# Performance work log

Measured on AMD Instinct MI355X. Metric: run time of the kernel, lower is better.

Reference implementation:

```python
import jax, jax.numpy as jnp
import numpy as np

B, S, D = 4, 2048, 1024
H = 8
HD = D // H            # 128 head dim
FF = 4096 // H         # 512 per-head expert hidden
E = 8                  # num experts
K = 2                  # top-k
MU, GAMMA = 0.7, 1.0
LN_EPS = 1e-5


def setup_inputs() -> dict:
    key = jax.random.key(0)
    ks = jax.random.split(key, 12)
    sc = lambda *shape: 1.0 / np.sqrt(shape[0])
    return {
        "x": jax.random.normal(ks[0], (B, S, D), jnp.float32),
        "momentum": jnp.zeros((B * S * H, HD), jnp.float32),
        # split proj (input_dim -> input_dim)
        "split_W": jax.random.normal(ks[1], (D, D), jnp.float32) * sc(D),
        "split_b": jnp.zeros((D,), jnp.float32),
        # gate (head_dim -> num_experts)
        "gate_W": jax.random.normal(ks[2], (HD, E), jnp.float32) * sc(HD),
        "gate_b": jnp.zeros((E,), jnp.float32),
        # stacked experts: Linear(HD->FF) ReLU Linear(FF->HD)
        "W1": jax.random.normal(ks[3], (E, HD, FF), jnp.float32) * sc(HD),
        "b1": jnp.zeros((E, FF), jnp.float32),
        "W2": jax.random.normal(ks[4], (E, FF, HD), jnp.float32) * sc(FF),
        "b2": jnp.zeros((E, HD), jnp.float32),
        # layernorm over head_dim
        "ln_g": jnp.ones((HD,), jnp.float32),
        "ln_b": jnp.zeros((HD,), jnp.float32),
        # merge proj
        "merge_W": jax.random.normal(ks[5], (D, D), jnp.float32) * sc(D),
        "merge_b": jnp.zeros((D,), jnp.float32),
    }


def _topk_gate(t, gate_W, gate_b):
    # t: [T, HD] -> dense gate weights [T, E] with only top-K nonzero
    logits = t @ gate_W + gate_b                       # [T, E]
    topv, topi = jax.lax.top_k(logits, K)              # [T, K]
    gates_k = jax.nn.softmax(topv, axis=-1)            # softmax over kept experts
    onehot = jax.nn.one_hot(topi, E, dtype=t.dtype)    # [T, K, E]
    return jnp.einsum("tk,tke->te", gates_k, onehot)   # scatter back


def reference(x, momentum, split_W, split_b, gate_W, gate_b,
              W1, b1, W2, b2, ln_g, ln_b, merge_W, merge_b):
    # split: [B,S,D] -> [B*S*H, HD]
    x_hat = x @ split_W + split_b
    t = x_hat.reshape(B * S * H, HD)

    gates = _topk_gate(t, gate_W, gate_b)              # [T, E]

    # all-experts dense compute (matches the source's per-expert loop)
    h = jax.nn.relu(jnp.einsum("td,edf->etf", t, W1) + b1[:, None, :])  # [E,T,FF]
    eo = jnp.einsum("etf,efd->etd", h, W2) + b2[:, None, :]             # [E,T,HD]
    expert_outputs = jnp.einsum("te,etd->td", gates, eo)                # [T,HD]

    new_momentum = -expert_outputs + MU * momentum
    out = t + GAMMA * new_momentum

    # layernorm over head_dim
    mean = out.mean(-1, keepdims=True)
    var = out.var(-1, keepdims=True)
    out = (out - mean) * jax.lax.rsqrt(var + LN_EPS) * ln_g + ln_b

    # merge: [T,HD] -> [B,S,D] -> linear
    o = out.reshape(B, S, D)
    final = o @ merge_W + merge_b
    return final, new_momentum
```

## Files before the change

kernel.cpp:

```cpp
#include <hip/hip_runtime.h>

#define NBATCH 4
#define NS 2048
#define ND 1024
#define NH 8
#define HD 128
#define NFF 512
#define NE 8
#define NT 65536
#define NBS 8192
#define MU_F 0.7f
#define LN_EPS_F 1e-5f

typedef __attribute__((ext_vector_type(4))) float f32x4;
typedef __attribute__((ext_vector_type(2))) double f64x2;
typedef __attribute__((ext_vector_type(8))) _Float16 f16x8;
typedef __attribute__((ext_vector_type(4))) _Float16 f16x4;
typedef __attribute__((ext_vector_type(2))) _Float16 f16x2;

__device__ __forceinline__ void gload_lds16(const void* g, void* l) {
  __builtin_amdgcn_global_load_lds(
      (const __attribute__((address_space(1))) unsigned int*)g,
      (__attribute__((address_space(3))) unsigned int*)l, 16, 0, 0);
}

__global__ void zero_cnt_kernel(int* cnt) {
  cnt[threadIdx.x] = 0;
}

__global__ void tr_cvt_kernel(const float* __restrict__ in, _Float16* __restrict__ out, int R, int C) {
  __shared__ float tile[32][33];
  int b = blockIdx.z;
  const float* inp = in + (size_t)b * R * C;
  _Float16* outp = out + (size_t)b * R * C;
  int c = blockIdx.x * 32 + threadIdx.x;
  int r0 = blockIdx.y * 32;
  #pragma unroll
  for (int i = 0; i < 4; i++) {
    int r = r0 + threadIdx.y + i * 8;
    tile[threadIdx.y + i * 8][threadIdx.x] = inp[(size_t)r * C + c];
  }
  __syncthreads();
  int rr = r0 + threadIdx.x;
  #pragma unroll
  for (int i = 0; i < 4; i++) {
    int cc = blockIdx.x * 32 + threadIdx.y + i * 8;
    outp[(size_t)cc * R + rr] = (_Float16)tile[threadIdx.x][threadIdx.y + i * 8];
  }
}

__global__ void build_G_kernel(const float* __restrict__ split_W, const float* __restrict__ split_b,
                               const float* __restrict__ gate_W, const float* __restrict__ gate_b,
                               double* __restrict__ G, double* __restrict__ gbias) {
  int idx = blockIdx.x * 256 + threadIdx.x;
  int d = idx >> 6, o = idx & 63, h = o >> 3, e = o & 7;
  double acc = 0.0;
  const float* r0 = split_W + (size_t)d * ND + h * 128;
  #pragma unroll 4
  for (int j = 0; j < 128; j++)
    acc += (double)r0[j] * (double)gate_W[j * 8 + e];
  G[((size_t)(d >> 1) * 64 + o) * 2 + (d & 1)] = acc;
  if (idx < 64) {
    double bacc = 0.0;
    for (int j = 0; j < 128; j++)
      bacc += (double)split_b[h * 128 + j] * (double)gate_W[j * 8 + e];
    gbias[idx] = bacc + (double)gate_b[e];
  }
}

__global__ __launch_bounds__(256) void gate_kernel(const float* __restrict__ x,
    const f64x2* __restrict__ Gx2, const double* __restrict__ gbias,
    _Float16* __restrict__ x_h,
    float* __restrict__ tkw, int* __restrict__ lists, int* __restrict__ cnt) {
  __shared__ f64x2 Gs[32 * 64];
  __shared__ double xsd[16][66];
  __shared__ double lg[16 * 64];
  __shared__ int lcnt[8];
  __shared__ int lbase[8];
  int tid = threadIdx.x, lane = tid & 63, w = tid >> 6;
  int bs0 = blockIdx.x * 16;
  double acc[4];
  #pragma unroll
  for (int r = 0; r < 4; r++) acc[r] = 0.0;
  int xrow = tid >> 4, xc4 = tid & 15;
  const double* xr = &xsd[0][0] + (w * 4) * 66;
  if (tid < 8) lcnt[tid] = 0;

  for (int ch = 0; ch < 16; ch++) {
    __syncthreads();
    float4 xv4 = *(const float4*)(x + (size_t)(bs0 + xrow) * ND + ch * 64 + xc4 * 4);
    f64x2 xa = { (double)xv4.x, (double)xv4.y };
    f64x2 xb = { (double)xv4.z, (double)xv4.w };
    *(f64x2*)&xsd[xrow][xc4 * 4]     = xa;
    *(f64x2*)&xsd[xrow][xc4 * 4 + 2] = xb;
    f16x4 xh = { (_Float16)xv4.x, (_Float16)xv4.y, (_Float16)xv4.z, (_Float16)xv4.w };
    *(f16x4*)(x_h + (size_t)(bs0 + xrow) * ND + ch * 64 + xc4 * 4) = xh;
    #pragma unroll
    for (int j = 0; j < 8; j++) {
      int n = j * 256 + tid;
      gload_lds16(Gx2 + (size_t)ch * 2048 + n, Gs + n);
    }
    __syncthreads();
    #pragma unroll 4
    for (int kp = 0; kp < 32; kp++) {
      f64x2 g = Gs[kp * 64 + lane];
      #pragma unroll
      for (int r = 0; r < 4; r++) {
        f64x2 xv = *(const f64x2*)(xr + r * 66 + kp * 2);
        acc[r] += xv.x * g.x;
        acc[r] += xv.y * g.y;
      }
    }
  }
  double gb = gbias[lane];
  #pragma unroll
  for (int r = 0; r < 4; r++)
    lg[(w * 4 + r) * 64 + lane] = acc[r] + gb;
  __syncthreads();

  int i1 = 0, i2 = 0, token = 0, p1 = 0, p2 = 0;
  if (tid < 128) {
    int row = tid >> 3, h = tid & 7;
    const double* L = lg + row * 64 + h * 8;
    double v1 = L[0];
    #pragma unroll
    for (int e2 = 1; e2 < 8; e2++) if (L[e2] > v1) { v1 = L[e2]; i1 = e2; }
    i2 = -1; double v2 = -1e300;
    #pragma unroll
    for (int e2 = 0; e2 < 8; e2++) if (e2 != i1 && L[e2] > v2) { v2 = L[e2]; i2 = e2; }
    float ex = expf((float)(v2 - v1));
    float den = 1.f + ex;
    float g1 = 1.f / den, g2 = ex / den;
    token = (bs0 + row) * 8 + h;
    tkw[token * 2]     = g1;
    tkw[token * 2 + 1] = g2;
    p1 = atomicAdd(&lcnt[i1], 1);
    p2 = atomicAdd(&lcnt[i2], 1);
  }
  __syncthreads();
  if (tid < 8) lbase[tid] = atomicAdd(cnt + tid * 64, lcnt[tid]);
  __syncthreads();
  if (tid < 128) {
    lists[(size_t)i1 * NT + lbase[i1] + p1] = token * 2;
    lists[(size_t)i2 * NT + lbase[i2] + p2] = token * 2 + 1;
  }
}

__global__ __launch_bounds__(256) void gemm_f16_kernel(
    const _Float16* __restrict__ A, const _Float16* __restrict__ Bt,
    const float* __restrict__ bias, float* __restrict__ Cf, _Float16* __restrict__ Ch,
    int M, int N, int Kd) {
  __shared__ _Float16 As[128 * 32];
  __shared__ _Float16 Bs[128 * 32];
  int tid = threadIdx.x, lane = tid & 63, w = tid >> 6;
  int wr = w >> 1, wc = w & 1;
  int m0 = blockIdx.y * 128, n0 = blockIdx.x * 128;
  f32x4 acc[4][4];
  #pragma unroll
  for (int i = 0; i < 4; i++)
    #pragma unroll
    for (int j = 0; j < 4; j++) acc[i][j] = (f32x4){0.f, 0.f, 0.f, 0.f};
  int srow = lane >> 2, scol = (lane & 3) * 8;
  int fr = lane & 15, ko = (lane >> 4) * 8;
  const _Float16* Ag = A + (size_t)(m0 + srow) * Kd + scol;
  const _Float16* Bg = Bt + (size_t)(n0 + srow) * Kd + scol;

  for (int k0 = 0; k0 < Kd; k0 += 32) {
    #pragma unroll
    for (int j = 0; j < 2; j++) {
      int rb = (w * 2 + j) * 16;
      gload_lds16(Ag + (size_t)rb * Kd + k0, As + rb * 32);
      gload_lds16(Bg + (size_t)rb * Kd + k0, Bs + rb * 32);
    }
    __syncthreads();
    f16x8 af[4], bq[4];
    #pragma unroll
    for (int mi = 0; mi < 4; mi++) af[mi] = *(const f16x8*)(As + (wr * 64 + mi * 16 + fr) * 32 + ko);
    #pragma unroll
    for (int ni = 0; ni < 4; ni++) bq[ni] = *(const f16x8*)(Bs + (wc * 64 + ni * 16 + fr) * 32 + ko);
    __syncthreads();
    #pragma unroll
    for (int mi = 0; mi < 4; mi++)
      #pragma unroll
      for (int ni = 0; ni < 4; ni++)
        acc[mi][ni] = __builtin_amdgcn_mfma_f32_16x16x32_f16(af[mi], bq[ni], acc[mi][ni], 0, 0, 0);
  }
  int rbase = m0 + wr * 64 + ((lane >> 4) << 2);
  int cbase = n0 + wc * 64 + (lane & 15);
  #pragma unroll
  for (int mi = 0; mi < 4; mi++)
    #pragma unroll
    for (int ni = 0; ni < 4; ni++) {
      int cc = cbase + ni * 16;
      float bv = bias ? bias[cc] : 0.f;
      #pragma unroll
      for (int r = 0; r < 4; r++) {
        int rr = rbase + mi * 16 + r;
        float v = acc[mi][ni][r] + bv;
        if (Cf) Cf[(size_t)rr * N + cc] = v;
        if (Ch) Ch[(size_t)rr * N + cc] = (_Float16)v;
      }
    }
}

__global__ __launch_bounds__(512, 2) void expert_kernel(
    const _Float16* __restrict__ t_h, const _Float16* __restrict__ W1t, const _Float16* __restrict__ W2t,
    const float* __restrict__ b1, const float* __restrict__ b2,
    const int* __restrict__ cnt, const int* __restrict__ lists, const float* __restrict__ tkw,
    _Float16* __restrict__ slots) {
  int e = blockIdx.x & 7;
  int m0 = (blockIdx.x >> 3) * 128;
  int count = cnt[e * 64];
  if (m0 >= count) return;
  __shared__ _Float16 ring[3][64 * 128];
  __shared__ _Float16 h_s[128 * 64];
  __shared__ float b1s[NFF];
  __shared__ float b2s[HD];
  __shared__ int alist[128];
  __shared__ float aw[128];
  int tid = threadIdx.x, lane = tid & 63, w = tid >> 6;
  int wr = w >> 1, wc = w & 1;
  int fr = lane & 15, g = lane >> 4;

  if (tid < 128) {
    int idx = m0 + tid;
    int a = (idx < count) ? lists[(size_t)e * NT + idx] : -1;
    alist[tid] = a;
    aw[tid] = (a >= 0) ? tkw[a] : 0.f;
  }
  b1s[tid] = b1[e * NFF + tid];
  if (tid < 128) b2s[tid] = b2[e * HD + tid];
  __syncthreads();

  auto stage = [&](int p) {
    if (p >= 16) return;
    int ch = p >> 1;
    _Float16* dst = &ring[p % 3][0];
    if ((p & 1) == 0) {
      #pragma unroll
      for (int j = 0; j < 2; j++) {
        int n = j * 512 + tid;
        int r = n >> 4, gg = n & 15;
        int sg = gg ^ ((r >> 1) & 7);
        gload_lds16(W1t + (size_t)e * (NFF * HD) + (size_t)(ch * 64 + r) * HD + sg * 8, dst + n * 8);
      }
    } else {
      #pragma unroll
      for (int j = 0; j < 2; j++) {
        int n = j * 512 + tid;
        int r = n >> 3, gg = n & 7;
        int sg = gg ^ ((r >> 1) & 7);
        gload_lds16(W2t + (size_t)e * (HD * NFF) + (size_t)r * NFF + ch * 64 + sg * 8, dst + n * 8);
      }
    }
  };

  f16x8 af[2][4];
  #pragma unroll
  for (int mi = 0; mi < 2; mi++) {
    int rloc = wr * 32 + mi * 16 + fr;
    int a = alist[rloc];
    const _Float16* tb = t_h + (size_t)(a >> 1) * HD;
    #pragma unroll
    for (int ks = 0; ks < 4; ks++) {
      f16x8 v = {0, 0, 0, 0, 0, 0, 0, 0};
      if (a >= 0) v = *(const f16x8*)(tb + ks * 32 + g * 8);
      af[mi][ks] = v;
    }
  }
  asm volatile("s_waitcnt vmcnt(0)" ::: "memory");
  stage(0); stage(1);
  asm volatile("s_waitcnt vmcnt(2) lgkmcnt(0)\n\ts_barrier" ::: "memory");

  f32x4 acc2[2][4];
  #pragma unroll
  for (int i = 0; i < 2; i++)
    #pragma unroll
    for (int j = 0; j < 4; j++) acc2[i][j] = (f32x4){0.f, 0.f, 0.f, 0.f};

  #pragma unroll
  for (int p = 0; p < 16; p++) {
    stage(p + 2);
    int ch = p >> 1;
    const char* WB = (const char*)&ring[p % 3][0];
    if ((p & 1) == 0) {
      float b1r[2][4];
      #pragma unroll
      for (int ni = 0; ni < 2; ni++)
        #pragma unroll
        for (int r = 0; r < 4; r++)
          b1r[ni][r] = b1s[ch * 64 + wc * 32 + ni * 16 + g * 4 + r];
      f32x4 acc1[2][2];
      #pragma unroll
      for (int i = 0; i < 2; i++)
        #pragma unroll
        for (int j = 0; j < 2; j++) acc1[i][j] = (f32x4){0.f, 0.f, 0.f, 0.f};
      #pragma unroll
      for (int ks = 0; ks < 4; ks++) {
        f16x8 bq[2];
        #pragma unroll
        for (int ni = 0; ni < 2; ni++) {
          int rw = wc * 32 + ni * 16 + fr;
          int byte = rw * 256 + ((ks * 64 + g * 16) ^ (((rw >> 1) & 7) << 4));
          bq[ni] = *(const f16x8*)(WB + byte);
        }
        #pragma unroll
        for (int mi = 0; mi < 2; mi++)
          #pragma unroll
          for (int ni = 0; ni < 2; ni++)
            acc1[mi][ni] = __builtin_amdgcn_mfma_f32_16x16x32_f16(bq[ni], af[mi][ks], acc1[mi][ni], 0, 0, 0);
      }
      #pragma unroll
      for (int mi = 0; mi < 2; mi++)
        #pragma unroll
        for (int ni = 0; ni < 2; ni++) {
          f16x4 hv;
          #pragma unroll
          for (int r = 0; r < 4; r++)
            hv[r] = (_Float16)fmaxf(acc1[mi][ni][r] + b1r[ni][r], 0.f);
          int tok = wr * 32 + mi * 16 + fr;
          int foff = wc * 64 + ni * 32 + g * 8;
          int byte = tok * 128 + (foff ^ (((tok >> 1) & 7) << 4));
          *(f16x4*)((char*)h_s + byte) = hv;
        }
    } else {
      #pragma unroll
      for (int ks = 0; ks < 2; ks++) {
        f16x8 ah[2], bq[4];
        #pragma unroll
        for (int mi = 0; mi < 2; mi++) {
          int row = wr * 32 + mi * 16 + fr;
          int byte = row * 128 + ((ks * 64 + g * 16) ^ (((row >> 1) & 7) << 4));
          ah[mi] = *(const f16x8*)((const char*)h_s + byte);
        }
        #pragma unroll
        for (int ni = 0; ni < 4; ni++) {
          int rw = wc * 64 + ni * 16 + fr;
          int byte = rw * 128 + ((ks * 64 + g * 16) ^ (((rw >> 1) & 7) << 4));
          bq[ni] = *(const f16x8*)((const char*)&ring[p % 3][0] + byte);
        }
        #pragma unroll
        for (int mi = 0; mi < 2; mi++)
          #pragma unroll
          for (int ni = 0; ni < 4; ni++)
            acc2[mi][ni] = __builtin_amdgcn_mfma_f32_16x16x32_f16(ah[mi], bq[ni], acc2[mi][ni], 0, 0, 0);
      }
    }
    if (p == 14) {
      asm volatile("s_waitcnt vmcnt(0) lgkmcnt(0)\n\ts_barrier" ::: "memory");
    } else if (p < 14) {
      asm volatile("s_waitcnt vmcnt(2) lgkmcnt(0)\n\ts_barrier" ::: "memory");
    }
  }
  #pragma unroll
  for (int mi = 0; mi < 2; mi++)
    #pragma unroll
    for (int ni = 0; ni < 4; ni++) {
      int ncol = wc * 64 + ni * 16 + fr;
      float bv = b2s[ncol];
      #pragma unroll
      for (int r = 0; r < 4; r++) {
        int m = wr * 32 + mi * 16 + g * 4 + r;
        int a = alist[m];
        if (a >= 0)
          slots[(size_t)a * HD + ncol] = (_Float16)(aw[m] * (acc2[mi][ni][r] + bv));
      }
    }
}

__global__ __launch_bounds__(256) void combine_ln_kernel(
    const _Float16* __restrict__ slots, const float* __restrict__ momentum,
    const _Float16* __restrict__ t_h, const float* __restrict__ ln_g, const float* __restrict__ ln_b,
    float* __restrict__ nm_out, _Float16* __restrict__ out_h) {
  int w = threadIdx.x >> 6, lane = threadIdx.x & 63;
  int tok = blockIdx.x * 4 + w;
  int d0 = lane * 2;
  f16x2 s0 = *(const f16x2*)(slots + (size_t)tok * 256 + d0);
  f16x2 s1 = *(const f16x2*)(slots + (size_t)tok * 256 + 128 + d0);
  float2 mo = *(const float2*)(momentum + (size_t)tok * HD + d0);
  f16x2 tv = *(const f16x2*)(t_h + (size_t)tok * HD + d0);
  float nm0 = -((float)s0.x + (float)s1.x) + MU_F * mo.x;
  float nm1 = -((float)s0.y + (float)s1.y) + MU_F * mo.y;
  float2 nm2; nm2.x = nm0; nm2.y = nm1;
  *(float2*)(nm_out + (size_t)tok * HD + d0) = nm2;
  float r0 = (float)tv.x + nm0;
  float r1 = (float)tv.y + nm1;
  float s = r0 + r1, sq = r0 * r0 + r1 * r1;
  #pragma unroll
  for (int m = 1; m < 64; m <<= 1) { s += __shfl_xor(s, m, 64); sq += __shfl_xor(sq, m, 64); }
  float mean = s * (1.f / 128.f);
  float var = sq * (1.f / 128.f) - mean * mean;
  float is = rsqrtf(var + LN_EPS_F);
  float y0 = (r0 - mean) * is * ln_g[d0] + ln_b[d0];
  float y1 = (r1 - mean) * is * ln_g[d0 + 1] + ln_b[d0 + 1];
  f16x2 yo = { (_Float16)y0, (_Float16)y1 };
  *(f16x2*)(out_h + (size_t)tok * HD + d0) = yo;
}

extern "C" void kernel_launch(void* const* d_in, const int* in_sizes, int n_in,
                              void* d_out, int out_size, void* d_ws, size_t ws_size,
                              hipStream_t stream) {
  const float* x        = (const float*)d_in[0];
  const float* momentum = (const float*)d_in[1];
  const float* split_W  = (const float*)d_in[2];
  const float* split_b  = (const float*)d_in[3];
  const float* gate_W   = (const float*)d_in[4];
  const float* gate_b   = (const float*)d_in[5];
  const float* W1       = (const float*)d_in[6];
  const float* b1       = (const float*)d_in[7];
  const float* W2       = (const float*)d_in[8];
  const float* b2       = (const float*)d_in[9];
  const float* ln_g     = (const float*)d_in[10];
  const float* ln_b     = (const float*)d_in[11];
  const float* merge_W  = (const float*)d_in[12];
  const float* merge_b  = (const float*)d_in[13];
  float* final_out = (float*)d_out;
  float* nm_out    = final_out + (size_t)NBS * ND;

  char* ws = (char*)d_ws;
  size_t off = 0;
  auto alloc = [&](size_t bytes) { void* p = ws + off; off = (off + bytes + 255) & ~(size_t)255; return p; };
  _Float16* x_h   = (_Float16*)alloc((size_t)NBS * ND * 2);
  _Float16* t_h   = (_Float16*)alloc((size_t)NT * HD * 2);
  _Float16* out_h = (_Float16*)alloc((size_t)NT * HD * 2);
  _Float16* sWt   = (_Float16*)alloc((size_t)ND * ND * 2);
  _Float16* mWt   = (_Float16*)alloc((size_t)ND * ND * 2);
  _Float16* W1t   = (_Float16*)alloc((size_t)NE * HD * NFF * 2);
  _Float16* W2t   = (_Float16*)alloc((size_t)NE * HD * NFF * 2);
  f64x2*    Gx2   = (f64x2*)alloc((size_t)512 * 64 * 16);
  double*   gbias = (double*)alloc(64 * 8);
  float*    tkw   = (float*)alloc((size_t)NT * 2 * 4);
  int*      lists = (int*)alloc((size_t)NE * NT * 4);
  int*      cnt   = (int*)alloc(512 * 4);
  _Float16* slots = (_Float16*)alloc((size_t)NT * 2 * HD * 2);
  (void)in_sizes; (void)n_in; (void)out_size; (void)ws_size;

  zero_cnt_kernel<<<1, 512, 0, stream>>>(cnt);
  tr_cvt_kernel<<<dim3(32, 32, 1), dim3(32, 8), 0, stream>>>(split_W, sWt, ND, ND);
  tr_cvt_kernel<<<dim3(32, 32, 1), dim3(32, 8), 0, stream>>>(merge_W, mWt, ND, ND);
  tr_cvt_kernel<<<dim3(16, 4, 8), dim3(32, 8), 0, stream>>>(W1, W1t, HD, NFF);
  tr_cvt_kernel<<<dim3(4, 16, 8), dim3(32, 8), 0, stream>>>(W2, W2t, NFF, HD);
  build_G_kernel<<<256, 256, 0, stream>>>(split_W, split_b, gate_W, gate_b, (double*)Gx2, gbias);
  gate_kernel<<<512, 256, 0, stream>>>(x, Gx2, gbias, x_h, tkw, lists, cnt);
  gemm_f16_kernel<<<dim3(8, 64), 256, 0, stream>>>(x_h, sWt, split_b, nullptr, t_h, NBS, ND, ND);
  expert_kernel<<<NE * 512, 512, 0, stream>>>(t_h, W1t, W2t, b1, b2, cnt, lists, tkw, slots);
  combine_ln_kernel<<<NT / 4, 256, 0, stream>>>(slots, momentum, t_h, ln_g, ln_b, nm_out, out_h);
  gemm_f16_kernel<<<dim3(8, 64), 256, 0, stream>>>(out_h, mWt, merge_b, final_out, nullptr, NBS, ND, ND);
}
```

Baseline: 240.2 us.

## Triple-buffer gate kernel loads, swizzle GEMM tiles per XCD, fold counter zeroing

The gate projection kernel is restructured into a triple-buffered pipeline with smaller K chunks. It prefetches x and G two chunks ahead using async LDS loads and hand-written waitcnt barriers, so global loads overlap the FP64 math. The GEMM block index is remapped so consecutive M tiles land on the same XCD to improve L2 reuse of the B operand. The counter zeroing kernel is folded into build_G to save a launch. The manual waitcnt counts are fragile if the number of outstanding loads changes.

```diff
diff --git a/kernel.cpp b/kernel.cpp
--- a/kernel.cpp
+++ b/kernel.cpp
@@ -24,10 +24,6 @@
       (__attribute__((address_space(3))) unsigned int*)l, 16, 0, 0);
 }
 
-__global__ void zero_cnt_kernel(int* cnt) {
-  cnt[threadIdx.x] = 0;
-}
-
 __global__ void tr_cvt_kernel(const float* __restrict__ in, _Float16* __restrict__ out, int R, int C) {
   __shared__ float tile[32][33];
   int b = blockIdx.z;
@@ -51,8 +47,10 @@
 
 __global__ void build_G_kernel(const float* __restrict__ split_W, const float* __restrict__ split_b,
                                const float* __restrict__ gate_W, const float* __restrict__ gate_b,
-                               double* __restrict__ G, double* __restrict__ gbias) {
+                               double* __restrict__ G, double* __restrict__ gbias,
+                               int* __restrict__ cnt) {
   int idx = blockIdx.x * 256 + threadIdx.x;
+  if (blockIdx.x == 0 && threadIdx.x < 256) { cnt[threadIdx.x] = 0; cnt[threadIdx.x + 256] = 0; }
   int d = idx >> 6, o = idx & 63, h = o >> 3, e = o & 7;
   double acc = 0.0;
   const float* r0 = split_W + (size_t)d * ND + h * 128;
@@ -72,8 +70,8 @@
     const f64x2* __restrict__ Gx2, const double* __restrict__ gbias,
     _Float16* __restrict__ x_h,
     float* __restrict__ tkw, int* __restrict__ lists, int* __restrict__ cnt) {
-  __shared__ f64x2 Gs[32 * 64];
-  __shared__ double xsd[16][66];
+  __shared__ f64x2 Gs[3][16 * 64];
+  __shared__ double xsd[3][16 * 34];
   __shared__ double lg[16 * 64];
   __shared__ int lcnt[8];
   __shared__ int lbase[8];
@@ -82,34 +80,51 @@
   double acc[4];
   #pragma unroll
   for (int r = 0; r < 4; r++) acc[r] = 0.0;
-  int xrow = tid >> 4, xc4 = tid & 15;
-  const double* xr = &xsd[0][0] + (w * 4) * 66;
   if (tid < 8) lcnt[tid] = 0;
 
-  for (int ch = 0; ch < 16; ch++) {
-    __syncthreads();
-    float4 xv4 = *(const float4*)(x + (size_t)(bs0 + xrow) * ND + ch * 64 + xc4 * 4);
-    f64x2 xa = { (double)xv4.x, (double)xv4.y };
-    f64x2 xb = { (double)xv4.z, (double)xv4.w };
-    *(f64x2*)&xsd[xrow][xc4 * 4]     = xa;
-    *(f64x2*)&xsd[xrow][xc4 * 4 + 2] = xb;
-    f16x4 xh = { (_Float16)xv4.x, (_Float16)xv4.y, (_Float16)xv4.z, (_Float16)xv4.w };
-    *(f16x4*)(x_h + (size_t)(bs0 + xrow) * ND + ch * 64 + xc4 * 4) = xh;
-    #pragma unroll
-    for (int j = 0; j < 8; j++) {
+  auto stageX = [&](int ch) {
+    if (tid < 128) {
+      int xrow = tid >> 3, c4 = tid & 7;
+      float4 xv4 = *(const float4*)(x + (size_t)(bs0 + xrow) * ND + ch * 32 + c4 * 4);
+      double* xd = &xsd[ch % 3][0] + xrow * 34 + c4 * 4;
+      f64x2 xa = { (double)xv4.x, (double)xv4.y };
+      f64x2 xb = { (double)xv4.z, (double)xv4.w };
+      *(f64x2*)xd = xa;
+      *(f64x2*)(xd + 2) = xb;
+      f16x4 xh = { (_Float16)xv4.x, (_Float16)xv4.y, (_Float16)xv4.z, (_Float16)xv4.w };
+      *(f16x4*)(x_h + (size_t)(bs0 + xrow) * ND + ch * 32 + c4 * 4) = xh;
+    }
+  };
+  auto stageG = [&](int ch) {
+    #pragma unroll
+    for (int j = 0; j < 4; j++) {
       int n = j * 256 + tid;
-      gload_lds16(Gx2 + (size_t)ch * 2048 + n, Gs + n);
-    }
-    __syncthreads();
+      gload_lds16(Gx2 + (size_t)ch * 1024 + n, &Gs[ch % 3][0] + n);
+    }
+  };
+
+  stageX(0); stageG(0);
+  stageX(1); stageG(1);
+  asm volatile("s_waitcnt vmcnt(4) lgkmcnt(0)\n\ts_barrier" ::: "memory");
+
+  for (int ch = 0; ch < 32; ch++) {
+    if (ch < 30) { stageX(ch + 2); stageG(ch + 2); }
+    const f64x2* Gc = &Gs[ch % 3][0];
+    const double* xr = &xsd[ch % 3][0] + (w * 4) * 34;
     #pragma unroll 4
-    for (int kp = 0; kp < 32; kp++) {
-      f64x2 g = Gs[kp * 64 + lane];
+    for (int kp = 0; kp < 16; kp++) {
+      f64x2 g = Gc[kp * 64 + lane];
       #pragma unroll
       for (int r = 0; r < 4; r++) {
-        f64x2 xv = *(const f64x2*)(xr + r * 66 + kp * 2);
+        f64x2 xv = *(const f64x2*)(xr + r * 34 + kp * 2);
         acc[r] += xv.x * g.x;
         acc[r] += xv.y * g.y;
       }
+    }
+    if (ch < 30) {
+      asm volatile("s_waitcnt vmcnt(4) lgkmcnt(0)\n\ts_barrier" ::: "memory");
+    } else {
+      asm volatile("s_waitcnt vmcnt(0) lgkmcnt(0)\n\ts_barrier" ::: "memory");
     }
   }
   double gb = gbias[lane];
@@ -154,7 +169,10 @@
   __shared__ _Float16 Bs[128 * 32];
   int tid = threadIdx.x, lane = tid & 63, w = tid >> 6;
   int wr = w >> 1, wc = w & 1;
-  int m0 = blockIdx.y * 128, n0 = blockIdx.x * 128;
+  int lid = blockIdx.y * 8 + blockIdx.x;
+  int xcd = lid & 7, sub = (lid >> 3) & 7, grp = lid >> 6;
+  int m0 = (xcd * 8 + sub) * 128;
+  int n0 = grp * 128;
   f32x4 acc[4][4];
   #pragma unroll
   for (int i = 0; i < 4; i++)
@@ -435,12 +453,11 @@
   _Float16* slots = (_Float16*)alloc((size_t)NT * 2 * HD * 2);
   (void)in_sizes; (void)n_in; (void)out_size; (void)ws_size;
 
-  zero_cnt_kernel<<<1, 512, 0, stream>>>(cnt);
   tr_cvt_kernel<<<dim3(32, 32, 1), dim3(32, 8), 0, stream>>>(split_W, sWt, ND, ND);
   tr_cvt_kernel<<<dim3(32, 32, 1), dim3(32, 8), 0, stream>>>(merge_W, mWt, ND, ND);
   tr_cvt_kernel<<<dim3(16, 4, 8), dim3(32, 8), 0, stream>>>(W1, W1t, HD, NFF);
   tr_cvt_kernel<<<dim3(4, 16, 8), dim3(32, 8), 0, stream>>>(W2, W2t, NFF, HD);
-  build_G_kernel<<<256, 256, 0, stream>>>(split_W, split_b, gate_W, gate_b, (double*)Gx2, gbias);
+  build_G_kernel<<<256, 256, 0, stream>>>(split_W, split_b, gate_W, gate_b, (double*)Gx2, gbias, cnt);
   gate_kernel<<<512, 256, 0, stream>>>(x, Gx2, gbias, x_h, tkw, lists, cnt);
   gemm_f16_kernel<<<dim3(8, 64), 256, 0, stream>>>(x_h, sWt, split_b, nullptr, t_h, NBS, ND, ND);
   expert_kernel<<<NE * 512, 512, 0, stream>>>(t_h, W1t, W2t, b1, b2, cnt, lists, tkw, slots);
```

Result: no change. 237.9 us (-1.0%).
